# Performance work log

Measured on AMD Instinct MI355X. Metric: run time of the kernel, lower is better.

The kernel has to match this reference:

```python
import jax, jax.numpy as jnp
import numpy as np

N_NODES = 100000
N_EDGES = 1600000
D_IN = 128
D_HID = 128
D_OUT = 128
ORIG = 90000


def setup_inputs() -> dict:
    key = jax.random.key(0)
    ks = jax.random.split(key, 8)
    x = jax.random.normal(ks[0], (N_NODES, D_IN), dtype=jnp.float32)
    edge_index = jax.random.randint(ks[1], (2, N_EDGES), 0, N_NODES, dtype=jnp.int64)
    # Glorot-ish scaled weights; PyG SAGEConv: lin_l (with bias) on aggregated, lin_r (no bias) on root
    s1 = 1.0 / np.sqrt(D_IN)
    s2 = 1.0 / np.sqrt(D_HID)
    Wl1 = jax.random.normal(ks[2], (D_IN, D_HID), dtype=jnp.float32) * s1
    bl1 = jnp.zeros((D_HID,), dtype=jnp.float32)
    Wr1 = jax.random.normal(ks[3], (D_IN, D_HID), dtype=jnp.float32) * s1
    Wl2 = jax.random.normal(ks[4], (D_HID, D_OUT), dtype=jnp.float32) * s2
    bl2 = jnp.zeros((D_OUT,), dtype=jnp.float32)
    Wr2 = jax.random.normal(ks[5], (D_HID, D_OUT), dtype=jnp.float32) * s2
    return {"x": x, "edge_index": edge_index, "original_size": ORIG,
            "Wl1": Wl1, "bl1": bl1, "Wr1": Wr1,
            "Wl2": Wl2, "bl2": bl2, "Wr2": Wr2}


def _sage_conv(x, src, dst, Wl, bl, Wr):
    # PyG SAGEConv (aggr='mean'): out = lin_l(mean_{j in N(i)} x_j) + lin_r(x_i)
    n = x.shape[0]
    msgs = x[src]                                            # [E, d] gather
    ssum = jax.ops.segment_sum(msgs, dst, num_segments=n)    # [N, d]
    cnt = jax.ops.segment_sum(jnp.ones((src.shape[0],), dtype=x.dtype), dst,
                              num_segments=n)                # [N]
    mean = ssum / jnp.maximum(cnt, 1.0)[:, None]             # 0 for isolated nodes
    return mean @ Wl + bl + x @ Wr


def reference(x, edge_index, original_size, Wl1, bl1, Wr1, Wl2, bl2, Wr2):
    src, dst = edge_index[0], edge_index[1]
    h = _sage_conv(x, src, dst, Wl1, bl1, Wr1)
    h = _sage_conv(h, src, dst, Wl2, bl2, Wr2)
    return h[:original_size]
```

## Files before the change

### kernel.cpp

```cpp
#include <hip/hip_runtime.h>

#define NN 100000
#define DD 128

typedef __attribute__((ext_vector_type(8))) short bf16x8;
typedef __attribute__((ext_vector_type(4))) float f32x4;
typedef __attribute__((ext_vector_type(2))) float f32x2;

__device__ __forceinline__ float bf2f(unsigned short u) {
    union { unsigned int i; float f; } v;
    v.i = ((unsigned int)u) << 16;
    return v.f;
}

__device__ __forceinline__ unsigned short f2bf(float f) {
    union { float f; unsigned int i; } v;
    v.f = f;
    unsigned int x = v.i;
    return (unsigned short)((x + 0x7FFFu + ((x >> 16) & 1u)) >> 16);
}

__device__ __forceinline__ float2 load2(const float* p, int i2) {
    return ((const float2*)p)[i2];
}

__device__ __forceinline__ f32x2 cvt2(unsigned int u) {
    union { unsigned int i; float f; } lo, hi;
    lo.i = u << 16;
    hi.i = u & 0xffff0000u;
    return (f32x2){lo.f, hi.f};
}

__device__ __forceinline__ bf16x8 load8_bf(const unsigned short* p) {
    return *((const bf16x8*)p);
}
__device__ __forceinline__ bf16x8 load8_bf(const float* p) {
    float4 a = ((const float4*)p)[0];
    float4 b = ((const float4*)p)[1];
    bf16x8 r;
    r[0] = (short)f2bf(a.x); r[1] = (short)f2bf(a.y);
    r[2] = (short)f2bf(a.z); r[3] = (short)f2bf(a.w);
    r[4] = (short)f2bf(b.x); r[5] = (short)f2bf(b.y);
    r[6] = (short)f2bf(b.z); r[7] = (short)f2bf(b.w);
    return r;
}


#define PCH 16
#define NBUKMAX 512
#define CAP 12288

__global__ __launch_bounds__(256) void hist_buckets(
    const int* __restrict__ ei, int E, int* __restrict__ bcnt, int nbuk) {
    __shared__ int is64_s;
    __shared__ int hl[NBUKMAX];
    int tid = threadIdx.x;
    for (int i = tid; i < nbuk; i += 256) hl[i] = 0;
    if (tid < 64) {
        int ok = (ei[2 * tid + 1] == 0);
        int all = __all(ok);
        if (tid == 0) is64_s = all;
    }
    __syncthreads();
    int is64 = is64_s;
    int e0 = blockIdx.x * (256 * PCH) + tid;
#pragma unroll
    for (int c = 0; c < PCH; c++) {
        int e = e0 + c * 256;
        if (e < E) {
            int d = is64 ? ei[2 * (E + e)] : ei[E + e];
            atomicAdd(&hl[d >> 8], 1);
        }
    }
    __syncthreads();
    for (int i = tid; i < nbuk; i += 256) {
        int v = hl[i];
        if (v) atomicAdd(&bcnt[i], v);
    }
}

__global__ void scan_buckets(const int* __restrict__ bcnt, int nbuk,
                             int* __restrict__ boff, int* __restrict__ offN, int E) {
    __shared__ int wsum[8];
    int tid = threadIdx.x;
    int lane = tid & 63, wid = tid >> 6;
    int v = (tid < nbuk) ? bcnt[tid] : 0;
    int s = v;
#pragma unroll
    for (int dl = 1; dl < 64; dl <<= 1) {
        int t = __shfl_up(s, dl, 64);
        if (lane >= dl) s += t;
    }
    if (lane == 63) wsum[wid] = s;
    __syncthreads();
    int w = 0;
#pragma unroll
    for (int i = 0; i < 8; i++) w += (i < wid) ? wsum[i] : 0;
    if (tid < nbuk) boff[tid] = w + s - v;
    if (tid == nbuk - 1) boff[nbuk] = w + s;
    if (tid == 0) offN[0] = E;
}

__global__ __launch_bounds__(256) void partition_edges(
    const int* __restrict__ ei, int E, const int* __restrict__ boff,
    int* __restrict__ bcur, unsigned long long* __restrict__ pairs, int nbuk) {
    __shared__ int is64_s;
    __shared__ int cntb[NBUKMAX];
    __shared__ int baseb[NBUKMAX];
    __shared__ int boffb[NBUKMAX];
    int tid = threadIdx.x;
    for (int i = tid; i < nbuk; i += 256) {
        cntb[i] = 0;
        boffb[i] = boff[i];
    }
    if (tid < 64) {
        int ok = (ei[2 * tid + 1] == 0);
        int all = __all(ok);
        if (tid == 0) is64_s = all;
    }
    __syncthreads();
    int is64 = is64_s;
    int e0 = blockIdx.x * (256 * PCH) + tid;

    int dv[PCH], sv[PCH], bl[PCH];
    bool va[PCH];
#pragma unroll
    for (int c = 0; c < PCH; c++) {
        int e = e0 + c * 256;
        va[c] = (e < E);
        dv[c] = va[c] ? (is64 ? ei[2 * (E + e)] : ei[E + e]) : 0;
        sv[c] = va[c] ? (is64 ? ei[2 * e] : ei[e]) : 0;
        bl[c] = 0;
    }
#pragma unroll
    for (int c = 0; c < PCH; c++) {
        if (va[c]) {
            int b = dv[c] >> 8;
            int l = atomicAdd(&cntb[b], 1);
            bl[c] = (b << 16) | l;
        }
    }
    __syncthreads();
    for (int i = tid; i < nbuk; i += 256) {
        int cb = cntb[i];
        baseb[i] = cb ? atomicAdd(&bcur[i], cb) : 0;
    }
    __syncthreads();
#pragma unroll
    for (int c = 0; c < PCH; c++) {
        if (va[c]) {
            int b = bl[c] >> 16, l = bl[c] & 0xffff;
            pairs[(size_t)(boffb[b] + baseb[b] + l)] =
                ((unsigned long long)(unsigned int)dv[c] << 32) | (unsigned int)sv[c];
        }
    }
}

__global__ __launch_bounds__(256) void build_csr(
    const unsigned long long* __restrict__ pairs, const int* __restrict__ boff,
    int* __restrict__ off, int* __restrict__ csr, int* __restrict__ cur, int N) {
    int b = blockIdx.x;
    int lo = b << 8;
    if (lo >= N) return;
    int hi = min(lo + 256, N);
    int nn = hi - lo;
    int base = boff[b];
    int pcount = boff[b + 1] - base;

    __shared__ int cnt_l[256];
    __shared__ int start_l[256];
    __shared__ int cur_l[256];
    __shared__ int wsum[4];
    __shared__ int lds_csr[CAP];

    int tid = threadIdx.x;
    cnt_l[tid] = 0;
    __syncthreads();

    for (int i = tid; i < pcount; i += 256) {
        int d = (int)(pairs[base + i] >> 32);
        atomicAdd(&cnt_l[d - lo], 1);
    }
    __syncthreads();

    int v = cnt_l[tid];
    int s = v;
    int lane = tid & 63, wid = tid >> 6;
#pragma unroll
    for (int dl = 1; dl < 64; dl <<= 1) {
        int t = __shfl_up(s, dl, 64);
        if (lane >= dl) s += t;
    }
    if (lane == 63) wsum[wid] = s;
    __syncthreads();
    int w = 0;
#pragma unroll
    for (int i = 0; i < 4; i++) w += (i < wid) ? wsum[i] : 0;
    int excl = w + s - v;
    start_l[tid] = excl;
    cur_l[tid] = excl;
    if (tid < nn) off[lo + tid] = base + excl;
    __syncthreads();

    if (pcount <= CAP) {
        for (int i = tid; i < pcount; i += 256) {
            unsigned long long p = pairs[base + i];
            int d = (int)(p >> 32) - lo;
            int pos = atomicAdd(&cur_l[d], 1);
            lds_csr[pos] = (int)(p & 0xffffffffu);
        }
        __syncthreads();
        for (int i = tid; i < pcount; i += 256) csr[base + i] = lds_csr[i];
    } else {
        for (int i = tid; i < pcount; i += 256) {
            unsigned long long p = pairs[base + i];
            int dg = (int)(p >> 32);
            int q = atomicAdd(&cur[dg], 1);
            csr[base + start_l[dg - lo] + q] = (int)(p & 0xffffffffu);
        }
    }
}

__global__ void cast_bf16(const float* __restrict__ in, unsigned short* __restrict__ out,
                          int n4) {
    int i = blockIdx.x * blockDim.x + threadIdx.x;
    if (i >= n4) return;
    float4 v = ((const float4*)in)[i];
    ushort4 o;
    o.x = f2bf(v.x); o.y = f2bf(v.y); o.z = f2bf(v.z); o.w = f2bf(v.w);
    ((ushort4*)out)[i] = o;
}

__global__ void prep_weights(const float* __restrict__ Wl1, const float* __restrict__ Wr1,
                             const float* __restrict__ Wl2, const float* __restrict__ Wr2,
                             unsigned short* __restrict__ Wt1, unsigned short* __restrict__ Wt2) {
    __shared__ float t[32][33];
    int which = blockIdx.x >> 4;
    const float* W = (which == 0) ? Wl1 : (which == 1) ? Wr1 : (which == 2) ? Wl2 : Wr2;
    unsigned short* Wt = (which < 2) ? Wt1 : Wt2;
    int koff = (which & 1) * 128;
    int b = blockIdx.x & 15;
    int bx = b & 3, by = b >> 2;
    int c = threadIdx.x & 31, r8 = threadIdx.x >> 5;
#pragma unroll
    for (int i = 0; i < 4; i++) {
        int r = r8 + i * 8;
        t[r][c] = W[(by * 32 + r) * 128 + bx * 32 + c];
    }
    __syncthreads();
#pragma unroll
    for (int i = 0; i < 4; i++) {
        int r = r8 + i * 8;
        int fi = bx * 32 + r;
        int kk = koff + by * 32 + c;
        int idx = ((fi >> 4) * 8 + (kk >> 5)) * 512 + ((kk >> 3) & 3) * 128
                + (fi & 15) * 8 + (kk & 7);
        Wt[idx] = f2bf(t[c][r]);
    }
}

#define ACC8(u) do { \
    acc[0] += cvt2((u).x); acc[1] += cvt2((u).y); \
    acc[2] += cvt2((u).z); acc[3] += cvt2((u).w); } while (0)

__global__ __launch_bounds__(256) void aggregate_bf(
    const unsigned short* __restrict__ feat,
    const int* __restrict__ off, const int* __restrict__ csr,
    unsigned short* __restrict__ mean, int N, const int* __restrict__ limp) {
    int lim = limp ? min(N, limp[0]) : N;
    int node = blockIdx.x * 4 + (threadIdx.x >> 6);
    if (node >= lim) return;
    int lane = threadIdx.x & 63;
    int e = lane >> 4, q = lane & 15;
    int s0 = off[node], s1 = off[node + 1];

    f32x2 acc[4];
#pragma unroll
    for (int t = 0; t < 4; t++) acc[t] = (f32x2){0.f, 0.f};

    for (int c0 = s0; c0 < s1; c0 += 64) {
        int cdeg = min(64, s1 - c0);
        int cr = (lane < cdeg) ? csr[c0 + lane] : 0;
        int nb = (cdeg + 15) >> 4;

        uint4 C0 = make_uint4(0, 0, 0, 0), C1 = C0, C2 = C0, C3 = C0;
        {
            int i0 = e, i1 = e + 4, i2 = e + 8, i3 = e + 12;
            int t0 = __shfl(cr, i0, 64), t1 = __shfl(cr, i1, 64),
                t2 = __shfl(cr, i2, 64), t3 = __shfl(cr, i3, 64);
            if (i0 < cdeg) C0 = *((const uint4*)(feat + (size_t)t0 * 128 + q * 8));
            if (i1 < cdeg) C1 = *((const uint4*)(feat + (size_t)t1 * 128 + q * 8));
            if (i2 < cdeg) C2 = *((const uint4*)(feat + (size_t)t2 * 128 + q * 8));
            if (i3 < cdeg) C3 = *((const uint4*)(feat + (size_t)t3 * 128 + q * 8));
        }
        for (int b = 1; b < nb; b++) {
            int i0 = b * 16 + e, i1 = i0 + 4, i2 = i0 + 8, i3 = i0 + 12;
            int t0 = __shfl(cr, i0, 64), t1 = __shfl(cr, i1, 64),
                t2 = __shfl(cr, i2, 64), t3 = __shfl(cr, i3, 64);
            uint4 N0 = make_uint4(0, 0, 0, 0), N1 = N0, N2 = N0, N3 = N0;
            if (i0 < cdeg) N0 = *((const uint4*)(feat + (size_t)t0 * 128 + q * 8));
            if (i1 < cdeg) N1 = *((const uint4*)(feat + (size_t)t1 * 128 + q * 8));
            if (i2 < cdeg) N2 = *((const uint4*)(feat + (size_t)t2 * 128 + q * 8));
            if (i3 < cdeg) N3 = *((const uint4*)(feat + (size_t)t3 * 128 + q * 8));
            ACC8(C0); ACC8(C1); ACC8(C2); ACC8(C3);
            C0 = N0; C1 = N1; C2 = N2; C3 = N3;
        }
        ACC8(C0); ACC8(C1); ACC8(C2); ACC8(C3);
    }

#pragma unroll
    for (int t = 0; t < 4; t++) {
        union { f32x2 v; double d; } a, b;
        a.v = acc[t];
        b.d = __shfl_xor(a.d, 16, 64); a.v += b.v;
        b.d = __shfl_xor(a.d, 32, 64); a.v += b.v;
        acc[t] = a.v;
    }

    int deg = s1 - s0;
    float inv = (deg > 0) ? (1.0f / (float)deg) : 0.0f;
    if (e == 0) {
        bf16x8 o;
#pragma unroll
        for (int t = 0; t < 4; t++) {
            o[2 * t]     = (short)f2bf(acc[t].x * inv);
            o[2 * t + 1] = (short)f2bf(acc[t].y * inv);
        }
        *((bf16x8*)(mean + (size_t)node * 128 + q * 8)) = o;
    }
}

__global__ void aggregate_f32(const float* __restrict__ feat,
                              const int* __restrict__ off, const int* __restrict__ csr,
                              unsigned short* __restrict__ mean, int N) {
    int node = blockIdx.x * (blockDim.x >> 6) + (threadIdx.x >> 6);
    if (node >= N) return;
    int lane = threadIdx.x & 63;
    int s0 = off[node], s1 = off[node + 1];
    float ax = 0.f, ay = 0.f;
    for (int j = s0; j < s1; j++) {
        int s = csr[j];
        float2 v = load2(feat, s * 64 + lane);
        ax += v.x; ay += v.y;
    }
    float inv = (s1 > s0) ? (1.0f / (float)(s1 - s0)) : 0.0f;
    unsigned int p = (unsigned int)f2bf(ax * inv) | ((unsigned int)f2bf(ay * inv) << 16);
    ((unsigned int*)mean)[node * 64 + lane] = p;
}

template <typename TA2, typename TO>
__global__ __launch_bounds__(256) void gemm_mfma(
    const unsigned short* __restrict__ A1, const TA2* __restrict__ A2,
    const unsigned short* __restrict__ Wt, const float* __restrict__ bias,
    TO* __restrict__ out, int Arows, int Nlimit, const int* __restrict__ origp) {
    int lim = Nlimit;
    if (origp) lim = min(lim, origp[0]);
    int n0 = blockIdx.x * 64;
    if (n0 >= lim) return;

    int tid = threadIdx.x;
    int lane = tid & 63;
    int wid = tid >> 6;
    int wm = wid >> 1, wn = wid & 1;
    int qd = lane >> 4, l16 = lane & 15;

    int r0 = min(n0 + wm * 32 + l16, Arows - 1);
    int r1 = min(n0 + wm * 32 + 16 + l16, Arows - 1);

    f32x4 acc[2][4];
#pragma unroll
    for (int a = 0; a < 2; a++)
#pragma unroll
        for (int b = 0; b < 4; b++) acc[a][b] = (f32x4){0.f, 0.f, 0.f, 0.f};

#pragma unroll
    for (int ks = 0; ks < 8; ks++) {
        int kb = (ks & 3) * 32;
        bf16x8 a0, a1;
        if (ks < 4) {
            a0 = load8_bf(A1 + (size_t)r0 * 128 + kb + qd * 8);
            a1 = load8_bf(A1 + (size_t)r1 * 128 + kb + qd * 8);
        } else {
            a0 = load8_bf(A2 + (size_t)r0 * 128 + kb + qd * 8);
            a1 = load8_bf(A2 + (size_t)r1 * 128 + kb + qd * 8);
        }
#pragma unroll
        for (int tn = 0; tn < 4; tn++) {
            int slot = (wn * 4 + tn) * 8 + ks;
            bf16x8 bfrag = *((const bf16x8*)(Wt + slot * 512 + lane * 8));
            acc[0][tn] = __builtin_amdgcn_mfma_f32_16x16x32_bf16(a0, bfrag, acc[0][tn], 0, 0, 0);
            acc[1][tn] = __builtin_amdgcn_mfma_f32_16x16x32_bf16(a1, bfrag, acc[1][tn], 0, 0, 0);
        }
    }

#pragma unroll
    for (int tn = 0; tn < 4; tn++) {
        int f = wn * 64 + tn * 16 + l16;
        float bv = bias[f];
#pragma unroll
        for (int tm = 0; tm < 2; tm++) {
#pragma unroll
            for (int r = 0; r < 4; r++) {
                int n = n0 + wm * 32 + tm * 16 + qd * 4 + r;
                if (n < lim) {
                    float val = acc[tm][tn][r] + bv;
                    if constexpr (__is_same(TO, float))
                        out[n * 128 + f] = val;
                    else
                        out[n * 128 + f] = f2bf(val);
                }
            }
        }
    }
}

extern "C" void kernel_launch(void* const* d_in, const int* in_sizes, int n_in,
                              void* d_out, int out_size, void* d_ws, size_t ws_size,
                              hipStream_t stream) {
    const float* x   = (const float*)d_in[0];
    const int*   ei  = (const int*)d_in[1];
    const int*   org = (const int*)d_in[2];
    const float* Wl1 = (const float*)d_in[3];
    const float* bl1 = (const float*)d_in[4];
    const float* Wr1 = (const float*)d_in[5];
    const float* Wl2 = (const float*)d_in[6];
    const float* bl2 = (const float*)d_in[7];
    const float* Wr2 = (const float*)d_in[8];
    float* out = (float*)d_out;

    const int N = in_sizes[0] / DD;
    const int E = in_sizes[1] / 2;

    size_t szFeat = (size_t)N * DD * 2;
    size_t szBase = 2 * szFeat
                  + 2 * 65536
                  + (size_t)N * 4 + 4096
                  + (size_t)(N + 1) * 4
                  + 4096
                  + (size_t)E * 4;
    bool big = ws_size >= szBase + szFeat + 4096;

    char* ws = (char*)d_ws;
    unsigned short* mean = (unsigned short*)ws;  ws += szFeat;
    unsigned short* h    = (unsigned short*)ws;  ws += szFeat;
    unsigned short* xb   = nullptr;
    if (big) { xb = (unsigned short*)ws; ws += szFeat; }
    unsigned short* Wt1 = (unsigned short*)ws;  ws += 65536;
    unsigned short* Wt2 = (unsigned short*)ws;  ws += 65536;
    int* cur  = (int*)ws;  ws += (size_t)N * 4;
    int* bcnt = (int*)ws;  ws += 2048;
    int* bcur = (int*)ws;  ws += 2048;
    int* off  = (int*)ws;  ws += (size_t)(N + 1) * 4;
    int* boff = (int*)ws;  ws += 4096;
    int* csr  = (int*)ws;

    unsigned long long* pairs = (unsigned long long*)mean;

    int nbuk = (N + 255) >> 8;
    int edgeGrid = (E + 256 * PCH - 1) / (256 * PCH);

    hipMemsetAsync(cur, 0, (size_t)N * 4 + 4096, stream);
    hist_buckets<<<edgeGrid, 256, 0, stream>>>(ei, E, bcnt, nbuk);
    scan_buckets<<<1, 512, 0, stream>>>(bcnt, nbuk, boff, off + N, E);
    partition_edges<<<edgeGrid, 256, 0, stream>>>(ei, E, boff, bcur, pairs, nbuk);
    build_csr<<<nbuk, 256, 0, stream>>>(pairs, boff, off, csr, cur, N);

    prep_weights<<<64, 256, 0, stream>>>(Wl1, Wr1, Wl2, Wr2, Wt1, Wt2);

    int aggGrid  = (N + 3) / 4;
    int gemmGrid = (N + 63) / 64;

    if (big) {
        cast_bf16<<<(N * DD / 4 + 255) / 256, 256, 0, stream>>>(x, xb, N * DD / 4);
        aggregate_bf<<<aggGrid, 256, 0, stream>>>(xb, off, csr, mean, N, nullptr);
        gemm_mfma<unsigned short, unsigned short><<<gemmGrid, 256, 0, stream>>>(
            mean, xb, Wt1, bl1, h, N, N, nullptr);
    } else {
        aggregate_f32<<<aggGrid, 256, 0, stream>>>(x, off, csr, mean, N);
        gemm_mfma<float, unsigned short><<<gemmGrid, 256, 0, stream>>>(
            mean, x, Wt1, bl1, h, N, N, nullptr);
    }
    aggregate_bf<<<aggGrid, 256, 0, stream>>>(h, off, csr, mean, N, org);
    gemm_mfma<unsigned short, float><<<gemmGrid, 256, 0, stream>>>(
        mean, h, Wt2, bl2, out, N, N, org);
}
```

Baseline: 330.9 us.

## Simplify aggregation gather loop, use packed bf16 convert, and remap GEMM warp tiling

The aggregation kernel drops its software-pipelined double-buffer loop in favour of full 16-neighbour batches with 32-bit byte offsets, plus a separately masked remainder batch. The mean output now uses v_cvt_pk_bf16_f32 in place of manual rounding. The GEMM kernel gives each wave 16 rows across all 128 output columns instead of a 32x64 tile, which removes the second A fragment. The aim is to cut address arithmetic and register pressure, at the cost of losing explicit load/compute overlap in the gather and of more weight-fragment loads per wave.

Result: slower. 361.0 us (+9.1%).

```diff
diff --git a/kernel.cpp b/kernel.cpp
--- a/kernel.cpp
+++ b/kernel.cpp
@@ -273,6 +273,8 @@
     int lane = threadIdx.x & 63;
     int e = lane >> 4, q = lane & 15;
     int s0 = off[node], s1 = off[node + 1];
+    unsigned qoff = (unsigned)q << 4;
+    const char* fb = (const char*)feat;
 
     f32x2 acc[4];
 #pragma unroll
@@ -281,31 +283,30 @@
     for (int c0 = s0; c0 < s1; c0 += 64) {
         int cdeg = min(64, s1 - c0);
         int cr = (lane < cdeg) ? csr[c0 + lane] : 0;
-        int nb = (cdeg + 15) >> 4;
-
-        uint4 C0 = make_uint4(0, 0, 0, 0), C1 = C0, C2 = C0, C3 = C0;
-        {
-            int i0 = e, i1 = e + 4, i2 = e + 8, i3 = e + 12;
-            int t0 = __shfl(cr, i0, 64), t1 = __shfl(cr, i1, 64),
-                t2 = __shfl(cr, i2, 64), t3 = __shfl(cr, i3, 64);
-            if (i0 < cdeg) C0 = *((const uint4*)(feat + (size_t)t0 * 128 + q * 8));
-            if (i1 < cdeg) C1 = *((const uint4*)(feat + (size_t)t1 * 128 + q * 8));
-            if (i2 < cdeg) C2 = *((const uint4*)(feat + (size_t)t2 * 128 + q * 8));
-            if (i3 < cdeg) C3 = *((const uint4*)(feat + (size_t)t3 * 128 + q * 8));
-        }
-        for (int b = 1; b < nb; b++) {
-            int i0 = b * 16 + e, i1 = i0 + 4, i2 = i0 + 8, i3 = i0 + 12;
-            int t0 = __shfl(cr, i0, 64), t1 = __shfl(cr, i1, 64),
-                t2 = __shfl(cr, i2, 64), t3 = __shfl(cr, i3, 64);
-            uint4 N0 = make_uint4(0, 0, 0, 0), N1 = N0, N2 = N0, N3 = N0;
-            if (i0 < cdeg) N0 = *((const uint4*)(feat + (size_t)t0 * 128 + q * 8));
-            if (i1 < cdeg) N1 = *((const uint4*)(feat + (size_t)t1 * 128 + q * 8));
-            if (i2 < cdeg) N2 = *((const uint4*)(feat + (size_t)t2 * 128 + q * 8));
-            if (i3 < cdeg) N3 = *((const uint4*)(feat + (size_t)t3 * 128 + q * 8));
+        int nfull = cdeg >> 4, rem = cdeg & 15;
+        for (int b = 0; b < nfull; b++) {
+            int i0 = b * 16 + e;
+            unsigned o0 = ((unsigned)__shfl(cr, i0, 64) << 8) + qoff;
+            unsigned o1 = ((unsigned)__shfl(cr, i0 + 4, 64) << 8) + qoff;
+            unsigned o2 = ((unsigned)__shfl(cr, i0 + 8, 64) << 8) + qoff;
+            unsigned o3 = ((unsigned)__shfl(cr, i0 + 12, 64) << 8) + qoff;
+            uint4 C0 = *(const uint4*)(fb + o0);
+            uint4 C1 = *(const uint4*)(fb + o1);
+            uint4 C2 = *(const uint4*)(fb + o2);
+            uint4 C3 = *(const uint4*)(fb + o3);
             ACC8(C0); ACC8(C1); ACC8(C2); ACC8(C3);
-            C0 = N0; C1 = N1; C2 = N2; C3 = N3;
-        }
-        ACC8(C0); ACC8(C1); ACC8(C2); ACC8(C3);
+        }
+        if (rem) {
+            int i0 = nfull * 16 + e;
+            int t0 = __shfl(cr, i0, 64), t1 = __shfl(cr, i0 + 4, 64),
+                t2 = __shfl(cr, i0 + 8, 64), t3 = __shfl(cr, i0 + 12, 64);
+            uint4 C0 = make_uint4(0, 0, 0, 0), C1 = C0, C2 = C0, C3 = C0;
+            if (i0 < cdeg)      C0 = *(const uint4*)(fb + ((((unsigned)t0) << 8) + qoff));
+            if (i0 + 4 < cdeg)  C1 = *(const uint4*)(fb + ((((unsigned)t1) << 8) + qoff));
+            if (i0 + 8 < cdeg)  C2 = *(const uint4*)(fb + ((((unsigned)t2) << 8) + qoff));
+            if (i0 + 12 < cdeg) C3 = *(const uint4*)(fb + ((((unsigned)t3) << 8) + qoff));
+            ACC8(C0); ACC8(C1); ACC8(C2); ACC8(C3);
+        }
     }
 
 #pragma unroll
@@ -320,13 +321,15 @@
     int deg = s1 - s0;
     float inv = (deg > 0) ? (1.0f / (float)deg) : 0.0f;
     if (e == 0) {
-        bf16x8 o;
-#pragma unroll
-        for (int t = 0; t < 4; t++) {
-            o[2 * t]     = (short)f2bf(acc[t].x * inv);
-            o[2 * t + 1] = (short)f2bf(acc[t].y * inv);
-        }
-        *((bf16x8*)(mean + (size_t)node * 128 + q * 8)) = o;
+        f32x2 iv = (f32x2){inv, inv};
+        f32x2 m0 = acc[0] * iv, m1 = acc[1] * iv,
+              m2 = acc[2] * iv, m3 = acc[3] * iv;
+        uint4 w;
+        asm("v_cvt_pk_bf16_f32 %0, %1, %2" : "=v"(w.x) : "v"(m0.x), "v"(m0.y));
+        asm("v_cvt_pk_bf16_f32 %0, %1, %2" : "=v"(w.y) : "v"(m1.x), "v"(m1.y));
+        asm("v_cvt_pk_bf16_f32 %0, %1, %2" : "=v"(w.z) : "v"(m2.x), "v"(m2.y));
+        asm("v_cvt_pk_bf16_f32 %0, %1, %2" : "=v"(w.w) : "v"(m3.x), "v"(m3.y));
+        *((uint4*)((char*)mean + (size_t)node * 256 + qoff)) = w;
     }
 }
 
@@ -361,54 +364,43 @@
     int tid = threadIdx.x;
     int lane = tid & 63;
     int wid = tid >> 6;
-    int wm = wid >> 1, wn = wid & 1;
     int qd = lane >> 4, l16 = lane & 15;
 
-    int r0 = min(n0 + wm * 32 + l16, Arows - 1);
-    int r1 = min(n0 + wm * 32 + 16 + l16, Arows - 1);
-
-    f32x4 acc[2][4];
-#pragma unroll
-    for (int a = 0; a < 2; a++)
-#pragma unroll
-        for (int b = 0; b < 4; b++) acc[a][b] = (f32x4){0.f, 0.f, 0.f, 0.f};
+    int r0 = min(n0 + wid * 16 + l16, Arows - 1);
+
+    f32x4 acc[8];
+#pragma unroll
+    for (int b = 0; b < 8; b++) acc[b] = (f32x4){0.f, 0.f, 0.f, 0.f};
 
 #pragma unroll
     for (int ks = 0; ks < 8; ks++) {
         int kb = (ks & 3) * 32;
-        bf16x8 a0, a1;
-        if (ks < 4) {
+        bf16x8 a0;
+        if (ks < 4)
             a0 = load8_bf(A1 + (size_t)r0 * 128 + kb + qd * 8);
-            a1 = load8_bf(A1 + (size_t)r1 * 128 + kb + qd * 8);
-        } else {
+        else
             a0 = load8_bf(A2 + (size_t)r0 * 128 + kb + qd * 8);
-            a1 = load8_bf(A2 + (size_t)r1 * 128 + kb + qd * 8);
-        }
-#pragma unroll
-        for (int tn = 0; tn < 4; tn++) {
-            int slot = (wn * 4 + tn) * 8 + ks;
+#pragma unroll
+        for (int tn = 0; tn < 8; tn++) {
+            int slot = tn * 8 + ks;
             bf16x8 bfrag = *((const bf16x8*)(Wt + slot * 512 + lane * 8));
-            acc[0][tn] = __builtin_amdgcn_mfma_f32_16x16x32_bf16(a0, bfrag, acc[0][tn], 0, 0, 0);
-            acc[1][tn] = __builtin_amdgcn_mfma_f32_16x16x32_bf16(a1, bfrag, acc[1][tn], 0, 0, 0);
-        }
-    }
-
-#pragma unroll
-    for (int tn = 0; tn < 4; tn++) {
-        int f = wn * 64 + tn * 16 + l16;
+            acc[tn] = __builtin_amdgcn_mfma_f32_16x16x32_bf16(a0, bfrag, acc[tn], 0, 0, 0);
+        }
+    }
+
+#pragma unroll
+    for (int tn = 0; tn < 8; tn++) {
+        int f = tn * 16 + l16;
         float bv = bias[f];
 #pragma unroll
-        for (int tm = 0; tm < 2; tm++) {
-#pragma unroll
-            for (int r = 0; r < 4; r++) {
-                int n = n0 + wm * 32 + tm * 16 + qd * 4 + r;
-                if (n < lim) {
-                    float val = acc[tm][tn][r] + bv;
-                    if constexpr (__is_same(TO, float))
-                        out[n * 128 + f] = val;
-                    else
-                        out[n * 128 + f] = f2bf(val);
-                }
+        for (int r = 0; r < 4; r++) {
+            int n = n0 + wid * 16 + qd * 4 + r;
+            if (n < lim) {
+                float val = acc[tn][r] + bv;
+                if constexpr (__is_same(TO, float))
+                    out[n * 128 + f] = val;
+                else
+                    out[n * 128 + f] = f2bf(val);
             }
         }
     }
```
